# Kernel optimization log

Hardware: AMD Instinct MI355X
Metric: run time of the kernel (lower is better)

Reference implementation:

```python
import jax, jax.numpy as jnp
import numpy as np

N = 4096
CIN = 128
COUT = 128
J = 2
DENSITY = 0.01  # ~40 nonzeros per Laplacian row


def _mask(k):
    m = (jax.random.uniform(k, (N, N)) < DENSITY).astype(jnp.float32)
    # Laplacians have nonzero diagonals; also guarantees no empty softmax rows
    return jnp.maximum(m, jnp.eye(N, dtype=jnp.float32))


def setup_inputs() -> dict:
    key = jax.random.key(0)
    ks = jax.random.split(key, 9)
    x = jax.random.normal(ks[0], (N, CIN), dtype=jnp.float32)
    Lup = _mask(ks[1])
    Ldown = _mask(ks[2])
    P = jax.random.normal(ks[3], (N, N), dtype=jnp.float32) / np.float32(np.sqrt(N))
    weight_irr = jax.random.normal(ks[4], (J, CIN, COUT), dtype=jnp.float32) * 0.05
    weight_sol = jax.random.normal(ks[5], (J, CIN, COUT), dtype=jnp.float32) * 0.05
    weight_har = jax.random.normal(ks[6], (CIN, COUT), dtype=jnp.float32) * 0.05
    att_irr = jax.random.normal(ks[7], (2 * J * COUT, 1), dtype=jnp.float32) * 0.05
    att_sol = jax.random.normal(ks[8], (2 * J * COUT, 1), dtype=jnp.float32) * 0.05
    return {"x": x, "Lup": Lup, "Ldown": Ldown, "P": P,
            "weight_irr": weight_irr, "weight_sol": weight_sol,
            "weight_har": weight_har, "att_irr": att_irr, "att_sol": att_sol}


def _masked_row_softmax(e, mask):
    # torch.sparse.softmax over the mask's nonzero pattern, dim=1, then to_dense
    on = mask > 0
    z = jnp.where(on, e, -jnp.inf)
    m = jnp.max(z, axis=1, keepdims=True)
    m = jnp.where(jnp.isfinite(m), m, 0.0)  # guard fully-masked rows
    p = jnp.exp(z - m)                      # exp(-inf)=0 off-pattern
    s = jnp.sum(p, axis=1, keepdims=True)
    s = jnp.where(s == 0, 1.0, s)
    return jnp.where(on, p / s, 0.0)


def _branch(x, weight, att, mask):
    j, cout = weight.shape[0], weight.shape[2]
    att_slice = j * cout
    h = jnp.einsum('ni,jio->jno', x, weight)         # [J, N, Cout]
    hf = h.reshape(-1, att_slice)                    # [N, J*Cout] (row-major, as torch)
    src = hf @ att[:att_slice]                       # [N, 1]
    dst = hf @ att[att_slice:]                       # [N, 1]
    e = jax.nn.leaky_relu(src + dst.T)               # [N, N], slope 0.01 (torch default)
    alpha = _masked_row_softmax(e, mask)             # [N, N]
    powers = [alpha]
    for _ in range(j - 1):
        powers.append(powers[-1] @ alpha)            # iterative matrix powers
    alpha_exp = jnp.stack(powers)                    # [J, N, N]
    # torch.sum with no dim: full reduction to a SCALAR (faithful to source)
    return jnp.sum(jnp.einsum('jnm,jmo->jno', alpha_exp, h))


def reference(x, Lup, Ldown, P, weight_irr, weight_sol, weight_har, att_irr, att_sol):
    z_irr = _branch(x, weight_irr, att_irr, Ldown)   # scalar
    z_sol = _branch(x, weight_sol, att_sol, Lup)     # scalar
    z_har = (P @ x) @ weight_har                     # [N, Cout]
    return z_irr + z_sol + z_har
```

## Files before the change

kernel.cpp:

```cpp
#include <hip/hip_runtime.h>

typedef __attribute__((ext_vector_type(8))) short short8b;
typedef __attribute__((ext_vector_type(4))) float f32x4;

#define NEG_SENTINEL (-1e30f)

constexpr int C_OFF    = 0;
constexpr int C2_OFF   = 8192;
constexpr int SC_OFF   = 16384;
constexpr int FLAG_I   = 16390;
constexpr int ZERO_N   = 16448;
constexpr int V_OFF    = 16448;
constexpr int NP_OFF   = 19008;
constexpr int SRC_OFF  = 100928;
constexpr int RM_OFF   = 117312;
constexpr int RS_OFF   = 125504;
constexpr int NNZ_OFF  = 133696;
constexpr int CCI_OFF  = 141888;
constexpr int XBT_OFF  = 666176;
constexpr int TP_OFF   = 928320;

__device__ __forceinline__ unsigned short f2bf(float f) {
  unsigned int u = __float_as_uint(f);
  u += 0x7FFFu + ((u >> 16) & 1u);
  return (unsigned short)(u >> 16);
}
__device__ __forceinline__ float bf2f(unsigned short b) {
  return __uint_as_float(((unsigned int)b) << 16);
}
__device__ __forceinline__ float scrub(float v) {
  unsigned int u = __float_as_uint(v);
  return ((u & 0x7F800000u) == 0x7F800000u) ? 0.f : v;
}

__global__ __launch_bounds__(256) void k_detect(const unsigned int* __restrict__ xw,
                                                int* __restrict__ flag) {
  int t = threadIdx.x;
  unsigned int ef = (xw[t] >> 7) & 0xFFu;
  int inb = (ef >= 100u && ef <= 150u) ? 1 : 0;
  __shared__ int s[256];
  s[t] = inb;
  __syncthreads();
  for (int d = 128; d > 0; d >>= 1) { if (t < d) s[t] += s[t + d]; __syncthreads(); }
  if (t == 0) *flag = (s[0] >= 192) ? 1 : 0;
}

__global__ __launch_bounds__(128) void k_vvec(const void* __restrict__ w_irr,
                                              const void* __restrict__ w_sol,
                                              const void* __restrict__ att_irr,
                                              const void* __restrict__ att_sol,
                                              const int* __restrict__ flag,
                                              float* __restrict__ vvec) {
  int f = *flag;
  int bx = blockIdx.x;
  int b = bx / 10, rem = bx % 10, j = rem / 5, tt = rem % 5;
  const void* Wv = (b == 0 ? w_irr : w_sol);
  const void* Av = (b == 0 ? att_irr : att_sol);
  int i = threadIdx.x;
  float s = 0.f;
  if (f) {
    const unsigned short* Wr = (const unsigned short*)Wv + (size_t)j * 16384 + (size_t)i * 128;
    const unsigned short* Ar = (const unsigned short*)Av + tt * 128;
    for (int o = 0; o < 128; o += 8) {
      uint4 wq = *(const uint4*)(Wr + o);
      unsigned int ww[4] = {wq.x, wq.y, wq.z, wq.w};
      float cf[8];
      if (tt < 4) {
        uint4 aq = *(const uint4*)(Ar + o);
        unsigned int aa[4] = {aq.x, aq.y, aq.z, aq.w};
#pragma unroll
        for (int u = 0; u < 4; ++u) {
          cf[2 * u] = bf2f((unsigned short)(aa[u] & 0xFFFFu));
          cf[2 * u + 1] = bf2f((unsigned short)(aa[u] >> 16));
        }
      } else {
#pragma unroll
        for (int e = 0; e < 8; ++e) cf[e] = 1.0f;
      }
#pragma unroll
      for (int u = 0; u < 4; ++u) {
        s += bf2f((unsigned short)(ww[u] & 0xFFFFu)) * cf[2 * u];
        s += bf2f((unsigned short)(ww[u] >> 16)) * cf[2 * u + 1];
      }
    }
  } else {
    const float* Wr = (const float*)Wv + (size_t)j * 16384 + (size_t)i * 128;
    const float* Ar = (const float*)Av + tt * 128;
    for (int o = 0; o < 128; o += 4) {
      float4 wq = *(const float4*)(Wr + o);
      float4 aq = {1.f, 1.f, 1.f, 1.f};
      if (tt < 4) aq = *(const float4*)(Ar + o);
      s += wq.x * aq.x + wq.y * aq.y + wq.z * aq.z + wq.w * aq.w;
    }
  }
  vvec[bx * 128 + i] = s;
}

__global__ __launch_bounds__(256) void k_prep(const void* __restrict__ xin,
                                              const int* __restrict__ flag,
                                              const float* __restrict__ vvec,
                                              unsigned short* __restrict__ xbT,
                                              float* __restrict__ np,
                                              float* __restrict__ srcdst) {
  __shared__ __align__(16) float ldsx[64 * 130];
  __shared__ __align__(16) float ldsv[2560];
  __shared__ float ldsp[4 * 1280];
  __shared__ float npl[1280];
  int f = *flag;
  int t = threadIdx.x, nb = blockIdx.x * 64;
  for (int q = 0; q < 16; ++q) {
    int idx = q * 256 + t;
    int row = idx >> 6, cp = idx & 63;
    float vx, vy;
    if (f) {
      unsigned int u = ((const unsigned int*)xin)[(size_t)(nb + row) * 64 + cp];
      vx = bf2f((unsigned short)(u & 0xFFFFu));
      vy = bf2f((unsigned short)(u >> 16));
    } else {
      float2 v = ((const float2*)xin)[(size_t)(nb + row) * 64 + cp];
      vx = v.x; vy = v.y;
    }
    ldsx[row * 130 + cp * 2] = vx;
    ldsx[row * 130 + cp * 2 + 1] = vy;
  }
  for (int q = 0; q < 10; ++q) { int idx = q * 256 + t; ldsv[idx] = vvec[idx]; }
  __syncthreads();
  for (int q = 0; q < 32; ++q) {
    int idx = q * 256 + t;
    int c = idx >> 6, n = idx & 63;
    xbT[(size_t)c * 4096 + nb + n] = f2bf(ldsx[n * 130 + c]);
  }
  int row = t & 63, qq = t >> 6, i0 = qq * 32;
  float acc[20];
#pragma unroll
  for (int k = 0; k < 20; ++k) acc[k] = 0.f;
  for (int i = i0; i < i0 + 32; i += 2) {
    float2 xv = *(const float2*)&ldsx[row * 130 + i];
#pragma unroll
    for (int k = 0; k < 20; ++k) {
      float2 vk = *(const float2*)&ldsv[k * 128 + i];
      acc[k] += xv.x * vk.x + xv.y * vk.y;
    }
  }
#pragma unroll
  for (int k = 0; k < 20; ++k) ldsp[qq * 1280 + row * 20 + k] = acc[k];
  __syncthreads();
  for (int rep = 0; rep < 5; ++rep) {
    int idx = rep * 256 + t;
    int k = idx >> 6, rr = idx & 63;
    float s = ldsp[rr * 20 + k] + ldsp[1280 + rr * 20 + k] +
              ldsp[2560 + rr * 20 + k] + ldsp[3840 + rr * 20 + k];
    npl[k * 64 + rr] = s;
    np[(size_t)k * 4096 + nb + rr] = s;
  }
  __syncthreads();
  {
    int b = t >> 7, j = (t >> 6) & 1, kind = (t >> 5) & 1, q = t & 31;
    int bl = q * 2;
    int r = j * 2048 + (nb >> 1) + q;
    int kidx = b * 10 + j * 5 + kind * 2;
    float val = npl[kidx * 64 + bl] + npl[(kidx + 1) * 64 + bl + 1];
    srcdst[b * 8192 + kind * 4096 + r] = val;
  }
}

__global__ __launch_bounds__(256) void k_scan(const void* __restrict__ Ldown,
                                              const void* __restrict__ Lup,
                                              float* __restrict__ ws) {
  int b = blockIdx.y, t = threadIdx.x;
  int wid = t >> 6, l = t & 63;
  int r = blockIdx.x * 4 + wid;
  int f = ((const int*)ws)[FLAG_I];
  const void* mask = b ? Lup : Ldown;
  unsigned short* cci = (unsigned short*)(ws + CCI_OFF) + (size_t)(b * 4096 + r) * 128;
  unsigned long long lt = (1ULL << l) - 1ULL;
  int run = 0;
  if (f) {
    const uint4* rp = (const uint4*)((const unsigned short*)mask + (size_t)r * 4096);
    uint4 cur = rp[l];
    for (int it = 0; it < 8; ++it) {
      uint4 nxt = {0, 0, 0, 0};
      if (it < 7) nxt = rp[(it + 1) * 64 + l];
      unsigned int wv[4] = {cur.x, cur.y, cur.z, cur.w};
      unsigned int hm = 0;
#pragma unroll
      for (int u = 0; u < 4; ++u) {
        hm |= (wv[u] & 0xFFFFu) ? (1u << (2 * u)) : 0u;
        hm |= (wv[u] >> 16) ? (1u << (2 * u + 1)) : 0u;
      }
      int mbase = (it * 64 + l) * 8;
#pragma unroll
      for (int j = 0; j < 8; ++j) {
        unsigned long long bj = __ballot((hm >> j) & 1u);
        if ((hm >> j) & 1u) {
          int slot = run + (int)__popcll(bj & lt);
          if (slot < 128) cci[slot] = (unsigned short)(mbase + j);
        }
        run += (int)__popcll(bj);
      }
      cur = nxt;
    }
  } else {
    const uint4* rp = (const uint4*)((const float*)mask + (size_t)r * 4096);
    uint4 cur = rp[l];
    for (int it = 0; it < 16; ++it) {
      uint4 nxt = {0, 0, 0, 0};
      if (it < 15) nxt = rp[(it + 1) * 64 + l];
      unsigned int wv[4] = {cur.x, cur.y, cur.z, cur.w};
      unsigned int hm = 0;
#pragma unroll
      for (int u = 0; u < 4; ++u) hm |= wv[u] ? (1u << u) : 0u;
      int mbase = (it * 64 + l) * 4;
#pragma unroll
      for (int j = 0; j < 4; ++j) {
        unsigned long long bj = __ballot((hm >> j) & 1u);
        if ((hm >> j) & 1u) {
          int slot = run + (int)__popcll(bj & lt);
          if (slot < 128) cci[slot] = (unsigned short)(mbase + j);
        }
        run += (int)__popcll(bj);
      }
      cur = nxt;
    }
  }
  int nz = min(run, 128);
  if (l == 0) ((int*)ws)[NNZ_OFF + b * 4096 + r] = nz;
  __builtin_amdgcn_s_waitcnt(0);
  const float* srcp = ws + SRC_OFF + b * 8192;
  const float* dstp = srcp + 4096;
  float srcr = srcp[r];
  int m0 = (l < nz) ? (int)cci[l] : -1;
  int m1 = (64 + l < nz) ? (int)cci[64 + l] : -1;
  float e0 = NEG_SENTINEL, e1 = NEG_SENTINEL;
  if (m0 >= 0) { float e = srcr + dstp[m0]; e0 = (e >= 0.f) ? e : 0.01f * e; }
  if (m1 >= 0) { float e = srcr + dstp[m1]; e1 = (e >= 0.f) ? e : 0.01f * e; }
  float mx = fmaxf(e0, e1);
  float sm = ((m0 >= 0) ? __expf(e0 - mx) : 0.f) + ((m1 >= 0) ? __expf(e1 - mx) : 0.f);
  for (int d = 1; d < 64; d <<= 1) {
    float om = __shfl_xor(mx, d);
    float os = __shfl_xor(sm, d);
    float M = fmaxf(mx, om);
    sm = sm * __expf(mx - M) + os * __expf(om - M);
    mx = M;
  }
  if (l == 0) {
    ws[RM_OFF + b * 4096 + r] = mx;
    ws[RS_OFF + b * 4096 + r] = sm;
  }
  float inv = 1.0f / sm;
  if (m0 >= 0) atomicAdd(&ws[C_OFF + b * 4096 + m0], __expf(e0 - mx) * inv);
  if (m1 >= 0) atomicAdd(&ws[C_OFF + b * 4096 + m1], __expf(e1 - mx) * inv);
}

__device__ __forceinline__ float alpha_of(const float* ws, int b, int r, int m) {
  const float* srcp = ws + SRC_OFF + b * 8192;
  float e = srcp[r] + srcp[4096 + m];
  e = (e >= 0.f) ? e : 0.01f * e;
  return __expf(e - ws[RM_OFF + b * 4096 + r]) / ws[RS_OFF + b * 4096 + r];
}

__global__ __launch_bounds__(256) void k_c2(float* __restrict__ ws) {
  int b = blockIdx.y;
  int s = blockIdx.x * 256 + threadIdx.x;
  int r = s >> 7, k = s & 127;
  int nz = ((const int*)ws)[NNZ_OFF + b * 4096 + r];
  if (k < nz) {
    int m = ((const unsigned short*)(ws + CCI_OFF))[(size_t)(b * 4096 + r) * 128 + k];
    atomicAdd(&ws[C2_OFF + b * 4096 + m], ws[C_OFF + b * 4096 + r] * alpha_of(ws, b, r, m));
  }
}

__global__ __launch_bounds__(256) void k_scalar(float* __restrict__ ws) {
  int b = blockIdx.x, t = threadIdx.x;
  const float* cb  = ws + C_OFF  + b * 4096;
  const float* c2b = ws + C2_OFF + b * 4096;
  const float* hr0 = ws + NP_OFF + (b * 10 + 4) * 4096;
  const float* hr1 = ws + NP_OFF + (b * 10 + 9) * 4096;
  double acc = 0.0;
  for (int m = t; m < 4096; m += 256)
    acc += (double)scrub(cb[m]) * (double)scrub(hr0[m]) +
           (double)scrub(c2b[m]) * (double)scrub(hr1[m]);
  __shared__ double sd[256];
  sd[t] = acc;
  __syncthreads();
  for (int s = 128; s > 0; s >>= 1) { if (t < s) sd[t] += sd[t + s]; __syncthreads(); }
  if (t == 0) atomicAdd(&ws[SC_OFF], (float)sd[0]);
}

__global__ __launch_bounds__(256) void k_gemm1(const void* __restrict__ P,
                                               const unsigned short* __restrict__ xbT,
                                               const int* __restrict__ flag,
                                               float* __restrict__ TP) {
  __shared__ __align__(16) unsigned short a_lds[64 * 40];
  __shared__ __align__(16) unsigned short b_lds[128 * 40];
  int f = *flag;
  const int mt = blockIdx.x & 63, ks = blockIdx.x >> 6;
  const int mb = mt * 64;
  const int t = threadIdx.x;
  const int w = t >> 6, l = t & 63, quad = l >> 4, lr = l & 15;
  f32x4 acc[8] = {};
  const int arow = t >> 2, akq = (t & 3) << 3;
  const int bn = t >> 1, bh = (t & 1) << 4;
  const int k0 = ks * 512;
  uint4 aU, bU0, bU1;
#define LOADT(IT)                                                              \
  {                                                                            \
    const int kb = k0 + (IT) * 32;                                             \
    if (f) {                                                                   \
      aU = *(const uint4*)((const unsigned short*)P +                          \
                           (size_t)(mb + arow) * 4096 + kb + akq);             \
    } else {                                                                   \
      const float* pa = (const float*)P + (size_t)(mb + arow) * 4096 + kb + akq; \
      float4 f0 = *(const float4*)pa;                                          \
      float4 f1 = *(const float4*)(pa + 4);                                    \
      unsigned short u[8] = {f2bf(f0.x), f2bf(f0.y), f2bf(f0.z), f2bf(f0.w),   \
                             f2bf(f1.x), f2bf(f1.y), f2bf(f1.z), f2bf(f1.w)};  \
      aU = *(const uint4*)u;                                                   \
    }                                                                          \
    const unsigned short* src = xbT + (size_t)bn * 4096 + kb + bh;             \
    bU0 = *(const uint4*)src;                                                  \
    bU1 = *(const uint4*)(src + 8);                                            \
  }
  LOADT(0);
  for (int it = 0; it < 16; ++it) {
    *(uint4*)&a_lds[arow * 40 + akq] = aU;
    *(uint4*)&b_lds[bn * 40 + bh] = bU0;
    *(uint4*)&b_lds[bn * 40 + bh + 8] = bU1;
    __syncthreads();
    if (it < 15) LOADT(it + 1);
    short8b af = *(short8b*)&a_lds[(w * 16 + lr) * 40 + quad * 8];
#pragma unroll
    for (int nt = 0; nt < 8; ++nt) {
      short8b bf = *(short8b*)&b_lds[(nt * 16 + lr) * 40 + quad * 8];
      acc[nt] = __builtin_amdgcn_mfma_f32_16x16x32_bf16(af, bf, acc[nt], 0, 0, 0);
    }
    if (it < 15) __syncthreads();
  }
#undef LOADT
  float* Tp = TP + (size_t)ks * 524288;
#pragma unroll
  for (int nt = 0; nt < 8; ++nt)
#pragma unroll
    for (int rr = 0; rr < 4; ++rr) {
      int row = mb + w * 16 + quad * 4 + rr;
      int col = nt * 16 + lr;
      Tp[(size_t)row * 128 + col] = acc[nt][rr];
    }
}

__global__ __launch_bounds__(256) void k_gemm2(const float* __restrict__ TP,
                                               const void* __restrict__ W,
                                               const float* __restrict__ ws,
                                               void* __restrict__ outv) {
  __shared__ float tl[32 * 128];
  int f = ((const int*)ws)[FLAG_I];
  int t = threadIdx.x;
  int rb = blockIdx.x * 32;
  for (int q = 0; q < 4; ++q) {
    int vi = q * 256 + t;
    size_t base = (size_t)rb * 128 + (size_t)vi * 4;
    float4 s = {0.f, 0.f, 0.f, 0.f};
#pragma unroll
    for (int p = 0; p < 8; ++p) {
      float4 v = *(const float4*)&TP[(size_t)p * 524288 + base];
      s.x += v.x; s.y += v.y; s.z += v.z; s.w += v.w;
    }
    *(float4*)&tl[vi * 4] = s;
  }
  __syncthreads();
  int col = t & 127, rg = t >> 7;
  int r0 = rg * 16;
  float acc[16] = {};
  for (int k = 0; k < 128; k += 4) {
    float w0, w1, w2, w3;
    if (f) {
      const unsigned short* W16 = (const unsigned short*)W;
      w0 = bf2f(W16[(k + 0) * 128 + col]); w1 = bf2f(W16[(k + 1) * 128 + col]);
      w2 = bf2f(W16[(k + 2) * 128 + col]); w3 = bf2f(W16[(k + 3) * 128 + col]);
    } else {
      const float* W32 = (const float*)W;
      w0 = W32[(k + 0) * 128 + col]; w1 = W32[(k + 1) * 128 + col];
      w2 = W32[(k + 2) * 128 + col]; w3 = W32[(k + 3) * 128 + col];
    }
#pragma unroll
    for (int rr = 0; rr < 16; ++rr) {
      float4 tv = *(const float4*)&tl[(r0 + rr) * 128 + k];
      acc[rr] += tv.x * w0 + tv.y * w1 + tv.z * w2 + tv.w * w3;
    }
  }
  float s = scrub(ws[SC_OFF]);
#pragma unroll
  for (int rr = 0; rr < 16; ++rr) {
    size_t oi = (size_t)(rb + r0 + rr) * 128 + col;
    float v = s + acc[rr];
    if (f) ((unsigned short*)outv)[oi] = f2bf(v);
    else   ((float*)outv)[oi] = v;
  }
}

extern "C" void kernel_launch(void* const* d_in, const int* in_sizes, int n_in,
                              void* d_out, int out_size, void* d_ws, size_t ws_size,
                              hipStream_t stream) {
  const void* x       = d_in[0];
  const void* Lup     = d_in[1];
  const void* Ldown   = d_in[2];
  const void* P       = d_in[3];
  const void* w_irr   = d_in[4];
  const void* w_sol   = d_in[5];
  const void* w_har   = d_in[6];
  const void* att_irr = d_in[7];
  const void* att_sol = d_in[8];
  float* ws = (float*)d_ws;

  hipMemsetAsync(d_ws, 0, (size_t)ZERO_N * sizeof(float), stream);
  k_detect<<<1, 256, 0, stream>>>((const unsigned int*)x, (int*)ws + FLAG_I);
  k_vvec  <<<20, 128, 0, stream>>>(w_irr, w_sol, att_irr, att_sol,
                                   (int*)ws + FLAG_I, ws + V_OFF);
  k_prep  <<<64, 256, 0, stream>>>(x, (int*)ws + FLAG_I, ws + V_OFF,
                                   (unsigned short*)(ws + XBT_OFF), ws + NP_OFF,
                                   ws + SRC_OFF);
  k_gemm1 <<<512, 256, 0, stream>>>(P, (const unsigned short*)(ws + XBT_OFF),
                                    (int*)ws + FLAG_I, ws + TP_OFF);
  k_scan  <<<dim3(1024, 2), 256, 0, stream>>>(Ldown, Lup, ws);
  k_c2    <<<dim3(2048, 2), 256, 0, stream>>>(ws);
  k_scalar<<<2, 256, 0, stream>>>(ws);
  k_gemm2 <<<128, 256, 0, stream>>>(ws + TP_OFF, w_har, ws, d_out);
}
```

Baseline: 330.2 us.

## Fuse dtype detection into vvec, rework mask scan, halve gemm2 row tile

Removes the separate k_detect launch by having every k_vvec block recompute the dtype flag from the first 128 words of x, with block 0 writing it out. k_scan now issues all mask row loads up front into registers, builds a per-lane 64-bit nonzero bitmap, and computes compaction offsets with one prefix scan instead of one ballot per bit. The softmax loop then walks each lane's set bits using an online max and sum. k_gemm2 uses 16-row tiles over 256 blocks instead of 32-row tiles over 128 blocks, trading more blocks for fewer registers per thread. The sampled flag threshold changes from 192 of 256 to 96 of 128, and lanes with many nonzeros will be serialized in the new bit-walking loops.

```diff
diff --git a/kernel.cpp b/kernel.cpp
--- a/kernel.cpp
+++ b/kernel.cpp
@@ -33,30 +33,26 @@
   return ((u & 0x7F800000u) == 0x7F800000u) ? 0.f : v;
 }
 
-__global__ __launch_bounds__(256) void k_detect(const unsigned int* __restrict__ xw,
-                                                int* __restrict__ flag) {
-  int t = threadIdx.x;
-  unsigned int ef = (xw[t] >> 7) & 0xFFu;
-  int inb = (ef >= 100u && ef <= 150u) ? 1 : 0;
-  __shared__ int s[256];
-  s[t] = inb;
-  __syncthreads();
-  for (int d = 128; d > 0; d >>= 1) { if (t < d) s[t] += s[t + d]; __syncthreads(); }
-  if (t == 0) *flag = (s[0] >= 192) ? 1 : 0;
-}
-
-__global__ __launch_bounds__(128) void k_vvec(const void* __restrict__ w_irr,
+__global__ __launch_bounds__(128) void k_vvec(const void* __restrict__ xin,
+                                              const void* __restrict__ w_irr,
                                               const void* __restrict__ w_sol,
                                               const void* __restrict__ att_irr,
                                               const void* __restrict__ att_sol,
-                                              const int* __restrict__ flag,
+                                              int* __restrict__ flagp,
                                               float* __restrict__ vvec) {
-  int f = *flag;
+  __shared__ int sdet[128];
+  int t = threadIdx.x;
+  unsigned int ef = (((const unsigned int*)xin)[t] >> 7) & 0xFFu;
+  sdet[t] = (ef >= 100u && ef <= 150u) ? 1 : 0;
+  __syncthreads();
+  for (int d = 64; d > 0; d >>= 1) { if (t < d) sdet[t] += sdet[t + d]; __syncthreads(); }
+  int f = (sdet[0] >= 96) ? 1 : 0;
+  if (blockIdx.x == 0 && t == 0) *flagp = f;
   int bx = blockIdx.x;
   int b = bx / 10, rem = bx % 10, j = rem / 5, tt = rem % 5;
   const void* Wv = (b == 0 ? w_irr : w_sol);
   const void* Av = (b == 0 ? att_irr : att_sol);
-  int i = threadIdx.x;
+  int i = t;
   float s = 0.f;
   if (f) {
     const unsigned short* Wr = (const unsigned short*)Wv + (size_t)j * 16384 + (size_t)i * 128;
@@ -164,6 +160,11 @@
   }
 }
 
+__device__ __forceinline__ int col_of(int f, int l, int bit) {
+  if (f) return ((bit >> 3) * 512) + l * 8 + (bit & 7);
+  return ((bit >> 5) * 2048) + (((bit >> 2) & 7) * 256) + l * 4 + (bit & 3);
+}
+
 __global__ __launch_bounds__(256) void k_scan(const void* __restrict__ Ldown,
                                               const void* __restrict__ Lup,
                                               float* __restrict__ ws) {
@@ -171,71 +172,62 @@
   int wid = t >> 6, l = t & 63;
   int r = blockIdx.x * 4 + wid;
   int f = ((const int*)ws)[FLAG_I];
-  const void* mask = b ? Lup : Ldown;
   unsigned short* cci = (unsigned short*)(ws + CCI_OFF) + (size_t)(b * 4096 + r) * 128;
-  unsigned long long lt = (1ULL << l) - 1ULL;
-  int run = 0;
+  unsigned long long hm = 0ULL;
   if (f) {
-    const uint4* rp = (const uint4*)((const unsigned short*)mask + (size_t)r * 4096);
-    uint4 cur = rp[l];
+    const uint4* rp = (const uint4*)((const unsigned short*)(b ? Lup : Ldown) +
+                                     (size_t)r * 4096) + l;
+    uint4 cs[8];
+#pragma unroll
+    for (int it = 0; it < 8; ++it) cs[it] = rp[it * 64];
+#pragma unroll
     for (int it = 0; it < 8; ++it) {
-      uint4 nxt = {0, 0, 0, 0};
-      if (it < 7) nxt = rp[(it + 1) * 64 + l];
-      unsigned int wv[4] = {cur.x, cur.y, cur.z, cur.w};
-      unsigned int hm = 0;
+      unsigned int wv[4] = {cs[it].x, cs[it].y, cs[it].z, cs[it].w};
 #pragma unroll
       for (int u = 0; u < 4; ++u) {
-        hm |= (wv[u] & 0xFFFFu) ? (1u << (2 * u)) : 0u;
-        hm |= (wv[u] >> 16) ? (1u << (2 * u + 1)) : 0u;
+        hm |= ((unsigned long long)((wv[u] & 0xFFFFu) != 0u)) << (it * 8 + u * 2);
+        hm |= ((unsigned long long)((wv[u] >> 16) != 0u)) << (it * 8 + u * 2 + 1);
       }
-      int mbase = (it * 64 + l) * 8;
-#pragma unroll
-      for (int j = 0; j < 8; ++j) {
-        unsigned long long bj = __ballot((hm >> j) & 1u);
-        if ((hm >> j) & 1u) {
-          int slot = run + (int)__popcll(bj & lt);
-          if (slot < 128) cci[slot] = (unsigned short)(mbase + j);
-        }
-        run += (int)__popcll(bj);
+    }
+  } else {
+    const uint4* rp = (const uint4*)((const float*)(b ? Lup : Ldown) +
+                                     (size_t)r * 4096) + l;
+#pragma unroll
+    for (int p = 0; p < 2; ++p) {
+      uint4 cs[8];
+#pragma unroll
+      for (int it = 0; it < 8; ++it) cs[it] = rp[(p * 8 + it) * 64];
+#pragma unroll
+      for (int it = 0; it < 8; ++it) {
+        unsigned int wv[4] = {cs[it].x, cs[it].y, cs[it].z, cs[it].w};
+#pragma unroll
+        for (int u = 0; u < 4; ++u)
+          hm |= ((unsigned long long)(wv[u] != 0u)) << (p * 32 + it * 4 + u);
       }
-      cur = nxt;
-    }
-  } else {
-    const uint4* rp = (const uint4*)((const float*)mask + (size_t)r * 4096);
-    uint4 cur = rp[l];
-    for (int it = 0; it < 16; ++it) {
-      uint4 nxt = {0, 0, 0, 0};
-      if (it < 15) nxt = rp[(it + 1) * 64 + l];
-      unsigned int wv[4] = {cur.x, cur.y, cur.z, cur.w};
-      unsigned int hm = 0;
-#pragma unroll
-      for (int u = 0; u < 4; ++u) hm |= wv[u] ? (1u << u) : 0u;
-      int mbase = (it * 64 + l) * 4;
-#pragma unroll
-      for (int j = 0; j < 4; ++j) {
-        unsigned long long bj = __ballot((hm >> j) & 1u);
-        if ((hm >> j) & 1u) {
-          int slot = run + (int)__popcll(bj & lt);
-          if (slot < 128) cci[slot] = (unsigned short)(mbase + j);
-        }
-        run += (int)__popcll(bj);
-      }
-      cur = nxt;
-    }
-  }
-  int nz = min(run, 128);
-  if (l == 0) ((int*)ws)[NNZ_OFF + b * 4096 + r] = nz;
-  __builtin_amdgcn_s_waitcnt(0);
+    }
+  }
+  int cnt = __popcll(hm);
+  int pre = cnt;
+  for (int d = 1; d < 64; d <<= 1) {
+    int o = __shfl_up(pre, d);
+    if (l >= d) pre += o;
+  }
+  int base = pre - cnt;
+  int nz = __shfl(pre, 63);
+  if (l == 0) ((int*)ws)[NNZ_OFF + b * 4096 + r] = min(nz, 128);
   const float* srcp = ws + SRC_OFF + b * 8192;
   const float* dstp = srcp + 4096;
   float srcr = srcp[r];
-  int m0 = (l < nz) ? (int)cci[l] : -1;
-  int m1 = (64 + l < nz) ? (int)cci[64 + l] : -1;
-  float e0 = NEG_SENTINEL, e1 = NEG_SENTINEL;
-  if (m0 >= 0) { float e = srcr + dstp[m0]; e0 = (e >= 0.f) ? e : 0.01f * e; }
-  if (m1 >= 0) { float e = srcr + dstp[m1]; e1 = (e >= 0.f) ? e : 0.01f * e; }
-  float mx = fmaxf(e0, e1);
-  float sm = ((m0 >= 0) ? __expf(e0 - mx) : 0.f) + ((m1 >= 0) ? __expf(e1 - mx) : 0.f);
+  float mx = NEG_SENTINEL, sm = 0.f;
+  unsigned long long mm = hm;
+  while (mm) {
+    int bit = __builtin_ctzll(mm); mm &= mm - 1;
+    int m = col_of(f, l, bit);
+    float e = srcr + dstp[m];
+    e = (e >= 0.f) ? e : 0.01f * e;
+    if (e > mx) { sm = sm * __expf(mx - e) + 1.f; mx = e; }
+    else        { sm += __expf(e - mx); }
+  }
   for (int d = 1; d < 64; d <<= 1) {
     float om = __shfl_xor(mx, d);
     float os = __shfl_xor(sm, d);
@@ -248,8 +240,17 @@
     ws[RS_OFF + b * 4096 + r] = sm;
   }
   float inv = 1.0f / sm;
-  if (m0 >= 0) atomicAdd(&ws[C_OFF + b * 4096 + m0], __expf(e0 - mx) * inv);
-  if (m1 >= 0) atomicAdd(&ws[C_OFF + b * 4096 + m1], __expf(e1 - mx) * inv);
+  int slot = base;
+  mm = hm;
+  while (mm) {
+    int bit = __builtin_ctzll(mm); mm &= mm - 1;
+    int m = col_of(f, l, bit);
+    if (slot < 128) cci[slot] = (unsigned short)m;
+    ++slot;
+    float e = srcr + dstp[m];
+    e = (e >= 0.f) ? e : 0.01f * e;
+    atomicAdd(&ws[C_OFF + b * 4096 + m], __expf(e - mx) * inv);
+  }
 }
 
 __device__ __forceinline__ float alpha_of(const float* ws, int b, int r, int m) {
@@ -352,11 +353,11 @@
                                                const void* __restrict__ W,
                                                const float* __restrict__ ws,
                                                void* __restrict__ outv) {
-  __shared__ float tl[32 * 128];
+  __shared__ float tl[16 * 128];
   int f = ((const int*)ws)[FLAG_I];
   int t = threadIdx.x;
-  int rb = blockIdx.x * 32;
-  for (int q = 0; q < 4; ++q) {
+  int rb = blockIdx.x * 16;
+  for (int q = 0; q < 2; ++q) {
     int vi = q * 256 + t;
     size_t base = (size_t)rb * 128 + (size_t)vi * 4;
     float4 s = {0.f, 0.f, 0.f, 0.f};
@@ -369,8 +370,8 @@
   }
   __syncthreads();
   int col = t & 127, rg = t >> 7;
-  int r0 = rg * 16;
-  float acc[16] = {};
+  int r0 = rg * 8;
+  float acc[8] = {};
   for (int k = 0; k < 128; k += 4) {
     float w0, w1, w2, w3;
     if (f) {
@@ -383,14 +384,14 @@
       w2 = W32[(k + 2) * 128 + col]; w3 = W32[(k + 3) * 128 + col];
     }
 #pragma unroll
-    for (int rr = 0; rr < 16; ++rr) {
+    for (int rr = 0; rr < 8; ++rr) {
       float4 tv = *(const float4*)&tl[(r0 + rr) * 128 + k];
       acc[rr] += tv.x * w0 + tv.y * w1 + tv.z * w2 + tv.w * w3;
     }
   }
   float s = scrub(ws[SC_OFF]);
 #pragma unroll
-  for (int rr = 0; rr < 16; ++rr) {
+  for (int rr = 0; rr < 8; ++rr) {
     size_t oi = (size_t)(rb + r0 + rr) * 128 + col;
     float v = s + acc[rr];
     if (f) ((unsigned short*)outv)[oi] = f2bf(v);
@@ -413,8 +414,7 @@
   float* ws = (float*)d_ws;
 
   hipMemsetAsync(d_ws, 0, (size_t)ZERO_N * sizeof(float), stream);
-  k_detect<<<1, 256, 0, stream>>>((const unsigned int*)x, (int*)ws + FLAG_I);
-  k_vvec  <<<20, 128, 0, stream>>>(w_irr, w_sol, att_irr, att_sol,
+  k_vvec  <<<20, 128, 0, stream>>>(x, w_irr, w_sol, att_irr, att_sol,
                                    (int*)ws + FLAG_I, ws + V_OFF);
   k_prep  <<<64, 256, 0, stream>>>(x, (int*)ws + FLAG_I, ws + V_OFF,
                                    (unsigned short*)(ws + XBT_OFF), ws + NP_OFF,
@@ -424,5 +424,5 @@
   k_scan  <<<dim3(1024, 2), 256, 0, stream>>>(Ldown, Lup, ws);
   k_c2    <<<dim3(2048, 2), 256, 0, stream>>>(ws);
   k_scalar<<<2, 256, 0, stream>>>(ws);
-  k_gemm2 <<<128, 256, 0, stream>>>(ws + TP_OFF, w_har, ws, d_out);
-}
+  k_gemm2 <<<256, 256, 0, stream>>>(ws + TP_OFF, w_har, ws, d_out);
+}
```

Result: faster. 306.7 us (-7.1%).
